# Optimization experiments

Measured on AMD Instinct MI355X. Metric: run time of the kernel, lower is better.

The kernel has to match this reference:

```python
import jax, jax.numpy as jnp
import numpy as np

N_NODES = 100000
N_EDGES = 1000000
D_IN = 64
D_MODEL = 64  # H * D
H = 4
D = D_MODEL // H


def setup_inputs() -> dict:
    key = jax.random.key(0)
    ks = jax.random.split(key, 9)
    nodes = jax.random.normal(ks[0], (N_NODES, D_IN), dtype=jnp.float32)
    senders = jax.random.randint(ks[1], (N_EDGES,), 0, N_NODES, dtype=jnp.int32)
    receivers = jnp.sort(jax.random.randint(ks[2], (N_EDGES,), 0, N_NODES, dtype=jnp.int32))
    s = 1.0 / np.sqrt(D_IN)
    W_qk = jax.random.uniform(ks[3], (D_IN, D_MODEL), jnp.float32, -s, s)
    b_qk = jnp.zeros((D_MODEL,), jnp.float32)
    W_v = jax.random.uniform(ks[4], (D_IN, D_MODEL), jnp.float32, -s, s)
    b_v = jnp.zeros((D_MODEL,), jnp.float32)
    so = 1.0 / np.sqrt(D_MODEL)
    W_out = jax.random.uniform(ks[5], (D_MODEL, D_MODEL), jnp.float32, -so, so)
    b_out = jnp.zeros((D_MODEL,), jnp.float32)
    return {
        'nodes': nodes, 'W_qk': W_qk, 'b_qk': b_qk, 'W_v': W_v, 'b_v': b_v,
        'W_out': W_out, 'b_out': b_out, 'senders': senders, 'receivers': receivers,
    }


def _segment_softmax(logits, segment_ids, num_segments):
    # jraph-style numerically stable segment softmax (segments are sorted)
    maxs = jax.ops.segment_max(logits, segment_ids, num_segments, indices_are_sorted=True)
    e = jnp.exp(logits - maxs[segment_ids])
    z = jax.ops.segment_sum(e, segment_ids, num_segments, indices_are_sorted=True)
    return e / z[segment_ids]


def reference(nodes, W_qk, b_qk, W_v, b_v, W_out, b_out, senders, receivers):
    N = nodes.shape[0]
    # projections: N (H D) -> N H D
    qks = (nodes @ W_qk + b_qk).reshape(N, H, D)
    vs = (nodes @ W_v + b_v).reshape(N, H, D)
    # per-edge QK scores: [E, H]
    scores = jnp.einsum('ehd,ehd->eh', qks[receivers], qks[senders])
    attn = _segment_softmax(scores, receivers, N)
    # weighted message scatter: [E,H,D] -> [N, H*D]
    messages = (attn[..., None] * vs[senders]).reshape(-1, H * D)
    ctx = jax.ops.segment_sum(messages, receivers, N, indices_are_sorted=True)
    out = ctx @ W_out + b_out
    return out, attn
```

## Files before the change

### kernel.cpp

```cpp
#include <hip/hip_runtime.h>
#include <math.h>


#define XS_PAD 68
#define WS_PAD 132

typedef _Float16 h2 __attribute__((ext_vector_type(2)));

__device__ inline unsigned pack2(float a, float b) {
    h2 h = { (_Float16)a, (_Float16)b };
    return __builtin_bit_cast(unsigned, h);
}

__global__ __launch_bounds__(256) void mhga_proj_rowptr(
    const float* __restrict__ X,
    const float* __restrict__ Wqk, const float* __restrict__ bqk,
    const float* __restrict__ Wv,  const float* __restrict__ bv,
    unsigned char* __restrict__ packed,
    const int* __restrict__ receivers, int* __restrict__ row_ptr,
    int N, int E, int PB)
{
    if ((int)blockIdx.x >= PB) {
        const int n = (blockIdx.x - PB) * 256 + threadIdx.x;
        if (n > N) return;
        int lo = 0, hi = E;
        while (lo < hi) {
            const int mid = (lo + hi) >> 1;
            if (receivers[mid] < n) lo = mid + 1; else hi = mid;
        }
        row_ptr[n] = lo;
        return;
    }

    __shared__ float Xs[64 * XS_PAD];
    __shared__ float Ws[64 * WS_PAD];
    const int t = threadIdx.x;
    const int m0 = blockIdx.x * 64;

#pragma unroll
    for (int rep = 0; rep < 4; ++rep) {
        const int idx = t * 4 + rep * 1024;
        const int m = idx >> 6, k = idx & 63;
        float4 xv = make_float4(0.f, 0.f, 0.f, 0.f);
        if (m0 + m < N) xv = *(const float4*)(X + (size_t)(m0 + m) * 64 + k);
        Xs[(k + 0) * XS_PAD + m] = xv.x;
        Xs[(k + 1) * XS_PAD + m] = xv.y;
        Xs[(k + 2) * XS_PAD + m] = xv.z;
        Xs[(k + 3) * XS_PAD + m] = xv.w;
    }
#pragma unroll
    for (int rep = 0; rep < 8; ++rep) {
        const int idx = t * 4 + rep * 1024;
        const int k = idx >> 7, j = idx & 127;
        const float4 wv = (j < 64) ? *(const float4*)(Wqk + k * 64 + j)
                                   : *(const float4*)(Wv + k * 64 + (j - 64));
        *(float4*)(Ws + k * WS_PAD + j) = wv;
    }
    __syncthreads();

    const int tx = t & 15, ty = t >> 4;
    float acc[4][8] = {};
#pragma unroll 8
    for (int k = 0; k < 64; ++k) {
        const float4 a  = *(const float4*)(Xs + k * XS_PAD + ty * 4);
        const float4 b0 = *(const float4*)(Ws + k * WS_PAD + tx * 8);
        const float4 b1 = *(const float4*)(Ws + k * WS_PAD + tx * 8 + 4);
        const float av[4] = {a.x, a.y, a.z, a.w};
        const float bv8[8] = {b0.x, b0.y, b0.z, b0.w, b1.x, b1.y, b1.z, b1.w};
#pragma unroll
        for (int i = 0; i < 4; ++i)
#pragma unroll
            for (int j = 0; j < 8; ++j)
                acc[i][j] = fmaf(av[i], bv8[j], acc[i][j]);
    }

    const bool isV = (tx >= 8);
    const float* bias = isV ? bv : bqk;
    const int j0 = (tx & 7) * 8;
    const int c0 = (tx & 7) * 2;
    const float4 bb0 = *(const float4*)(bias + j0);
    const float4 bb1 = *(const float4*)(bias + j0 + 4);
#pragma unroll
    for (int i = 0; i < 4; ++i) {
        const int m = m0 + ty * 4 + i;
        if (m < N) {
            const unsigned u0 = pack2(acc[i][0] + bb0.x, acc[i][1] + bb0.y);
            const unsigned u1 = pack2(acc[i][2] + bb0.z, acc[i][3] + bb0.w);
            const unsigned u2 = pack2(acc[i][4] + bb1.x, acc[i][5] + bb1.y);
            const unsigned u3 = pack2(acc[i][6] + bb1.z, acc[i][7] + bb1.w);
            unsigned char* row = packed + (size_t)m * 256 + (isV ? 8 : 0);
            *(uint2*)(row + c0 * 16)       = make_uint2(u0, u1);
            *(uint2*)(row + (c0 + 1) * 16) = make_uint2(u2, u3);
        }
    }
}

__global__ __launch_bounds__(256) void mhga_attn(
    const unsigned char* __restrict__ packed,
    const int* __restrict__ senders, const int* __restrict__ row_ptr,
    const float* __restrict__ Wout, const float* __restrict__ bout,
    float* __restrict__ p_ws, float* __restrict__ out,
    float* __restrict__ attn_out, int N)
{
    __shared__ float sW[64 * 64];
    __shared__ float sCtx[4][64];
    const int t = threadIdx.x;
#pragma unroll
    for (int i = t * 4; i < 4096; i += 1024)
        *(float4*)(sW + i) = *(const float4*)(Wout + i);

    const int wave = t >> 6, lane = t & 63;
    const int g = lane >> 4, tl = lane & 15;
    const float bo = bout[lane];
    __syncthreads();

    for (int n0 = blockIdx.x * 4; n0 < N; n0 += gridDim.x * 4) {
        const int n = n0 + wave;
        const bool active = (n < N);
        float l = 0.f;
        float4 ctx = make_float4(0.f, 0.f, 0.f, 0.f);
        int e0 = 0, e1 = 0;

        if (active) {
            e0 = row_ptr[n];
            e1 = row_ptr[n + 1];
            const uint4 qpk = *(const uint4*)(packed + (size_t)n * 256 + tl * 16);
            const h2 q0 = __builtin_bit_cast(h2, qpk.x);
            const h2 q1 = __builtin_bit_cast(h2, qpk.y);

            for (int base = e0; base < e1; base += 64) {
                const int cnt = min(64, e1 - base);
                int sid = 0;
                if (base + lane < e1) sid = senders[base + lane];

                int idx = g;
                int scur = __shfl(sid, idx, 64);
                if (idx >= cnt) scur = 0;
                uint4 pk = *(const uint4*)(packed + (size_t)scur * 256 + tl * 16);

                const int iters = (cnt + 3) >> 2;
                for (int i = 0; i < iters; ++i) {
                    const int nidx = idx + 4;
                    int snxt = __shfl(sid, nidx & 63, 64);
                    if (nidx >= cnt) snxt = 0;
                    const uint4 pknext =
                        *(const uint4*)(packed + (size_t)snxt * 256 + tl * 16);
                    if (idx < cnt) {
                        const h2 k0 = __builtin_bit_cast(h2, pk.x);
                        const h2 k1 = __builtin_bit_cast(h2, pk.y);
                        const h2 v0 = __builtin_bit_cast(h2, pk.z);
                        const h2 v1 = __builtin_bit_cast(h2, pk.w);
                        float d = __builtin_amdgcn_fdot2(q0, k0, 0.f, false);
                        d = __builtin_amdgcn_fdot2(q1, k1, d, false);
                        d += __shfl_xor(d, 1, 64);
                        d += __shfl_xor(d, 2, 64);
                        const float p = __expf(d);
                        if ((tl & 3) == 0)
                            p_ws[(size_t)(base + idx) * 4 + (tl >> 2)] = p;
                        l += p;
                        ctx.x = fmaf(p, (float)v0.x, ctx.x);
                        ctx.y = fmaf(p, (float)v0.y, ctx.y);
                        ctx.z = fmaf(p, (float)v1.x, ctx.z);
                        ctx.w = fmaf(p, (float)v1.y, ctx.w);
                    }
                    pk = pknext;
                    idx = nidx;
                }
            }
#pragma unroll
            for (int mask = 16; mask <= 32; mask <<= 1) {
                l     += __shfl_xor(l, mask, 64);
                ctx.x += __shfl_xor(ctx.x, mask, 64);
                ctx.y += __shfl_xor(ctx.y, mask, 64);
                ctx.z += __shfl_xor(ctx.z, mask, 64);
                ctx.w += __shfl_xor(ctx.w, mask, 64);
            }
            const float inv = (l > 0.f) ? (1.f / l) : 0.f;
            if (g == 0) {
                *(float4*)(&sCtx[wave][tl * 4]) =
                    make_float4(ctx.x * inv, ctx.y * inv, ctx.z * inv, ctx.w * inv);
            }
        }

        __syncthreads();

        if (active) {
            const float lh = __shfl(l, (lane & 3) << 2, 64);
            const float invl = (lh > 0.f) ? (1.f / lh) : 0.f;
            volatile const float* vp = p_ws;
            for (int f = e0 * 4 + lane; f < e1 * 4; f += 64)
                attn_out[f] = vp[f] * invl;

            float acc = bo;
#pragma unroll
            for (int k = 0; k < 64; k += 4) {
                const float4 c = *(const float4*)(&sCtx[wave][k]);
                acc = fmaf(c.x, sW[(k + 0) * 64 + lane], acc);
                acc = fmaf(c.y, sW[(k + 1) * 64 + lane], acc);
                acc = fmaf(c.z, sW[(k + 2) * 64 + lane], acc);
                acc = fmaf(c.w, sW[(k + 3) * 64 + lane], acc);
            }
            out[(size_t)n * 64 + lane] = acc;
        }
    }
}

extern "C" void kernel_launch(void* const* d_in, const int* in_sizes, int n_in,
                              void* d_out, int out_size, void* d_ws, size_t ws_size,
                              hipStream_t stream) {
    const float* nodes   = (const float*)d_in[0];
    const float* W_qk    = (const float*)d_in[1];
    const float* b_qk    = (const float*)d_in[2];
    const float* W_v     = (const float*)d_in[3];
    const float* b_v     = (const float*)d_in[4];
    const float* W_out   = (const float*)d_in[5];
    const float* b_out   = (const float*)d_in[6];
    const int* senders   = (const int*)d_in[7];
    const int* receivers = (const int*)d_in[8];

    const int N = in_sizes[0] / 64;
    const int E = in_sizes[7];

    float* out      = (float*)d_out;
    float* attn_out = out + (size_t)N * 64;

    unsigned char* packed = (unsigned char*)d_ws;
    int*   rowp = (int*)(packed + (size_t)N * 256);
    float* p_ws = (float*)(rowp + (((N + 1) + 3) & ~3));

    const int PB = (N + 63) / 64;
    const int RB = (N + 1 + 255) / 256;
    mhga_proj_rowptr<<<PB + RB, 256, 0, stream>>>(
        nodes, W_qk, b_qk, W_v, b_v, packed, receivers, rowp, N, E, PB);

    mhga_attn<<<2048, 256, 0, stream>>>(packed, senders, rowp,
                                        W_out, b_out, p_ws, out, attn_out, N);
}
```

Measured before the change: 193.9 us.

## Use MFMA for node projection and drop block barrier in attention loop

Rewrites the projection GEMM to convert X and W to fp16 in swizzled shared memory and compute it with 16x16x32 f16 MFMA instructions instead of scalar FMAs. In the attention kernel, the per-iteration __syncthreads is replaced by a waitcnt so waves advance independently, and the software prefetch of the next sender row is removed in favour of a direct load. Inputs are now rounded to fp16 before the matmul, and the output is written with scattered 2-byte stores, so precision and store efficiency may change. Dropping the prefetch may expose more gather latency.

```diff
diff --git a/kernel.cpp b/kernel.cpp
--- a/kernel.cpp
+++ b/kernel.cpp
@@ -2,15 +2,11 @@
 #include <math.h>
 
 
-#define XS_PAD 68
-#define WS_PAD 132
-
 typedef _Float16 h2 __attribute__((ext_vector_type(2)));
-
-__device__ inline unsigned pack2(float a, float b) {
-    h2 h = { (_Float16)a, (_Float16)b };
-    return __builtin_bit_cast(unsigned, h);
-}
+typedef _Float16 half8 __attribute__((ext_vector_type(8)));
+typedef float floatx4 __attribute__((ext_vector_type(4)));
+
+#define WT_PAD 72
 
 __global__ __launch_bounds__(256) void mhga_proj_rowptr(
     const float* __restrict__ X,
@@ -32,8 +28,8 @@
         return;
     }
 
-    __shared__ float Xs[64 * XS_PAD];
-    __shared__ float Ws[64 * WS_PAD];
+    __shared__ __align__(16) _Float16 Xh[64 * WT_PAD];
+    __shared__ __align__(16) _Float16 Wt[128 * WT_PAD];
     const int t = threadIdx.x;
     const int m0 = blockIdx.x * 64;
 
@@ -43,10 +39,11 @@
         const int m = idx >> 6, k = idx & 63;
         float4 xv = make_float4(0.f, 0.f, 0.f, 0.f);
         if (m0 + m < N) xv = *(const float4*)(X + (size_t)(m0 + m) * 64 + k);
-        Xs[(k + 0) * XS_PAD + m] = xv.x;
-        Xs[(k + 1) * XS_PAD + m] = xv.y;
-        Xs[(k + 2) * XS_PAD + m] = xv.z;
-        Xs[(k + 3) * XS_PAD + m] = xv.w;
+        h2 lo = { (_Float16)xv.x, (_Float16)xv.y };
+        h2 hi = { (_Float16)xv.z, (_Float16)xv.w };
+        uint2 u = make_uint2(__builtin_bit_cast(unsigned, lo),
+                             __builtin_bit_cast(unsigned, hi));
+        *(uint2*)(&Xh[m * WT_PAD + k]) = u;
     }
 #pragma unroll
     for (int rep = 0; rep < 8; ++rep) {
@@ -54,43 +51,50 @@
         const int k = idx >> 7, j = idx & 127;
         const float4 wv = (j < 64) ? *(const float4*)(Wqk + k * 64 + j)
                                    : *(const float4*)(Wv + k * 64 + (j - 64));
-        *(float4*)(Ws + k * WS_PAD + j) = wv;
+        const float w4[4] = {wv.x, wv.y, wv.z, wv.w};
+#pragma unroll
+        for (int i = 0; i < 4; ++i) {
+            const int n = j + i;
+            Wt[n * WT_PAD + (k ^ ((n & 7) * 8))] = (_Float16)w4[i];
+        }
     }
     __syncthreads();
 
-    const int tx = t & 15, ty = t >> 4;
-    float acc[4][8] = {};
-#pragma unroll 8
-    for (int k = 0; k < 64; ++k) {
-        const float4 a  = *(const float4*)(Xs + k * XS_PAD + ty * 4);
-        const float4 b0 = *(const float4*)(Ws + k * WS_PAD + tx * 8);
-        const float4 b1 = *(const float4*)(Ws + k * WS_PAD + tx * 8 + 4);
-        const float av[4] = {a.x, a.y, a.z, a.w};
-        const float bv8[8] = {b0.x, b0.y, b0.z, b0.w, b1.x, b1.y, b1.z, b1.w};
-#pragma unroll
-        for (int i = 0; i < 4; ++i)
-#pragma unroll
-            for (int j = 0; j < 8; ++j)
-                acc[i][j] = fmaf(av[i], bv8[j], acc[i][j]);
-    }
-
-    const bool isV = (tx >= 8);
-    const float* bias = isV ? bv : bqk;
-    const int j0 = (tx & 7) * 8;
-    const int c0 = (tx & 7) * 2;
-    const float4 bb0 = *(const float4*)(bias + j0);
-    const float4 bb1 = *(const float4*)(bias + j0 + 4);
-#pragma unroll
-    for (int i = 0; i < 4; ++i) {
-        const int m = m0 + ty * 4 + i;
-        if (m < N) {
-            const unsigned u0 = pack2(acc[i][0] + bb0.x, acc[i][1] + bb0.y);
-            const unsigned u1 = pack2(acc[i][2] + bb0.z, acc[i][3] + bb0.w);
-            const unsigned u2 = pack2(acc[i][4] + bb1.x, acc[i][5] + bb1.y);
-            const unsigned u3 = pack2(acc[i][6] + bb1.z, acc[i][7] + bb1.w);
-            unsigned char* row = packed + (size_t)m * 256 + (isV ? 8 : 0);
-            *(uint2*)(row + c0 * 16)       = make_uint2(u0, u1);
-            *(uint2*)(row + (c0 + 1) * 16) = make_uint2(u2, u3);
+    const int w = t >> 6, lane = t & 63;
+    const int ln = lane & 15, quad = lane >> 4;
+
+    const half8 a0 = *(const half8*)(&Xh[(w * 16 + ln) * WT_PAD + quad * 8]);
+    const half8 a1 = *(const half8*)(&Xh[(w * 16 + ln) * WT_PAD + 32 + quad * 8]);
+
+    float bt[8];
+#pragma unroll
+    for (int tt = 0; tt < 8; ++tt)
+        bt[tt] = (tt < 4) ? bqk[tt * 16 + ln] : bv[(tt - 4) * 16 + ln];
+
+    floatx4 acc[8];
+#pragma unroll
+    for (int tt = 0; tt < 8; ++tt) {
+        const int n = tt * 16 + ln;
+        const int swz = (n & 7);
+        const half8 b0 = *(const half8*)(&Wt[n * WT_PAD + ((quad ^ swz) * 8)]);
+        const half8 b1 = *(const half8*)(&Wt[n * WT_PAD + (((4 + quad) ^ swz) * 8)]);
+        floatx4 c = {0.f, 0.f, 0.f, 0.f};
+        c = __builtin_amdgcn_mfma_f32_16x16x32_f16(a0, b0, c, 0, 0, 0);
+        c = __builtin_amdgcn_mfma_f32_16x16x32_f16(a1, b1, c, 0, 0, 0);
+        acc[tt] = c;
+    }
+
+#pragma unroll
+    for (int tt = 0; tt < 8; ++tt) {
+        const int off = (tt < 4)
+            ? ((tt * 4 + (ln >> 2)) * 16 + (ln & 3) * 2)
+            : (((tt - 4) * 4 + (ln >> 2)) * 16 + 8 + (ln & 3) * 2);
+#pragma unroll
+        for (int r = 0; r < 4; ++r) {
+            const int row = m0 + w * 16 + quad * 4 + r;
+            if (row < N)
+                *(_Float16*)(packed + (size_t)row * 256 + off) =
+                    (_Float16)(acc[tt][r] + bt[tt]);
         }
     }
 }
@@ -114,94 +118,77 @@
     const float bo = bout[lane];
     __syncthreads();
 
-    for (int n0 = blockIdx.x * 4; n0 < N; n0 += gridDim.x * 4) {
-        const int n = n0 + wave;
-        const bool active = (n < N);
+    for (int n = blockIdx.x * 4 + wave; n < N; n += gridDim.x * 4) {
+        const int e0 = row_ptr[n];
+        const int e1 = row_ptr[n + 1];
         float l = 0.f;
         float4 ctx = make_float4(0.f, 0.f, 0.f, 0.f);
-        int e0 = 0, e1 = 0;
-
-        if (active) {
-            e0 = row_ptr[n];
-            e1 = row_ptr[n + 1];
-            const uint4 qpk = *(const uint4*)(packed + (size_t)n * 256 + tl * 16);
-            const h2 q0 = __builtin_bit_cast(h2, qpk.x);
-            const h2 q1 = __builtin_bit_cast(h2, qpk.y);
-
-            for (int base = e0; base < e1; base += 64) {
-                const int cnt = min(64, e1 - base);
-                int sid = 0;
-                if (base + lane < e1) sid = senders[base + lane];
-
-                int idx = g;
-                int scur = __shfl(sid, idx, 64);
-                if (idx >= cnt) scur = 0;
-                uint4 pk = *(const uint4*)(packed + (size_t)scur * 256 + tl * 16);
-
-                const int iters = (cnt + 3) >> 2;
-                for (int i = 0; i < iters; ++i) {
-                    const int nidx = idx + 4;
-                    int snxt = __shfl(sid, nidx & 63, 64);
-                    if (nidx >= cnt) snxt = 0;
-                    const uint4 pknext =
-                        *(const uint4*)(packed + (size_t)snxt * 256 + tl * 16);
-                    if (idx < cnt) {
-                        const h2 k0 = __builtin_bit_cast(h2, pk.x);
-                        const h2 k1 = __builtin_bit_cast(h2, pk.y);
-                        const h2 v0 = __builtin_bit_cast(h2, pk.z);
-                        const h2 v1 = __builtin_bit_cast(h2, pk.w);
-                        float d = __builtin_amdgcn_fdot2(q0, k0, 0.f, false);
-                        d = __builtin_amdgcn_fdot2(q1, k1, d, false);
-                        d += __shfl_xor(d, 1, 64);
-                        d += __shfl_xor(d, 2, 64);
-                        const float p = __expf(d);
-                        if ((tl & 3) == 0)
-                            p_ws[(size_t)(base + idx) * 4 + (tl >> 2)] = p;
-                        l += p;
-                        ctx.x = fmaf(p, (float)v0.x, ctx.x);
-                        ctx.y = fmaf(p, (float)v0.y, ctx.y);
-                        ctx.z = fmaf(p, (float)v1.x, ctx.z);
-                        ctx.w = fmaf(p, (float)v1.y, ctx.w);
-                    }
-                    pk = pknext;
-                    idx = nidx;
+        const uint4 qpk = *(const uint4*)(packed + (size_t)n * 256 + tl * 16);
+        const h2 q0 = __builtin_bit_cast(h2, qpk.x);
+        const h2 q1 = __builtin_bit_cast(h2, qpk.y);
+
+        for (int base = e0; base < e1; base += 64) {
+            const int cnt = min(64, e1 - base);
+            int sid = 0;
+            if (base + lane < e1) sid = senders[base + lane];
+            const int iters = (cnt + 3) >> 2;
+            for (int i = 0; i < iters; ++i) {
+                const int idx = i * 4 + g;
+                const int s = __shfl(sid, idx, 64);
+                if (idx < cnt) {
+                    const uint4 pk =
+                        *(const uint4*)(packed + (size_t)s * 256 + tl * 16);
+                    const h2 k0 = __builtin_bit_cast(h2, pk.x);
+                    const h2 k1 = __builtin_bit_cast(h2, pk.y);
+                    const h2 v0 = __builtin_bit_cast(h2, pk.z);
+                    const h2 v1 = __builtin_bit_cast(h2, pk.w);
+                    float d = __builtin_amdgcn_fdot2(q0, k0, 0.f, false);
+                    d = __builtin_amdgcn_fdot2(q1, k1, d, false);
+                    d += __shfl_xor(d, 1, 64);
+                    d += __shfl_xor(d, 2, 64);
+                    const float p = __expf(d);
+                    if ((tl & 3) == 0)
+                        p_ws[(size_t)(base + idx) * 4 + (tl >> 2)] = p;
+                    l += p;
+                    ctx.x = fmaf(p, (float)v0.x, ctx.x);
+                    ctx.y = fmaf(p, (float)v0.y, ctx.y);
+                    ctx.z = fmaf(p, (float)v1.x, ctx.z);
+                    ctx.w = fmaf(p, (float)v1.y, ctx.w);
                 }
             }
-#pragma unroll
-            for (int mask = 16; mask <= 32; mask <<= 1) {
-                l     += __shfl_xor(l, mask, 64);
-                ctx.x += __shfl_xor(ctx.x, mask, 64);
-                ctx.y += __shfl_xor(ctx.y, mask, 64);
-                ctx.z += __shfl_xor(ctx.z, mask, 64);
-                ctx.w += __shfl_xor(ctx.w, mask, 64);
-            }
-            const float inv = (l > 0.f) ? (1.f / l) : 0.f;
-            if (g == 0) {
-                *(float4*)(&sCtx[wave][tl * 4]) =
-                    make_float4(ctx.x * inv, ctx.y * inv, ctx.z * inv, ctx.w * inv);
-            }
-        }
-
-        __syncthreads();
-
-        if (active) {
-            const float lh = __shfl(l, (lane & 3) << 2, 64);
-            const float invl = (lh > 0.f) ? (1.f / lh) : 0.f;
-            volatile const float* vp = p_ws;
-            for (int f = e0 * 4 + lane; f < e1 * 4; f += 64)
-                attn_out[f] = vp[f] * invl;
-
-            float acc = bo;
-#pragma unroll
-            for (int k = 0; k < 64; k += 4) {
-                const float4 c = *(const float4*)(&sCtx[wave][k]);
-                acc = fmaf(c.x, sW[(k + 0) * 64 + lane], acc);
-                acc = fmaf(c.y, sW[(k + 1) * 64 + lane], acc);
-                acc = fmaf(c.z, sW[(k + 2) * 64 + lane], acc);
-                acc = fmaf(c.w, sW[(k + 3) * 64 + lane], acc);
-            }
-            out[(size_t)n * 64 + lane] = acc;
-        }
+        }
+#pragma unroll
+        for (int mask = 16; mask <= 32; mask <<= 1) {
+            l     += __shfl_xor(l, mask, 64);
+            ctx.x += __shfl_xor(ctx.x, mask, 64);
+            ctx.y += __shfl_xor(ctx.y, mask, 64);
+            ctx.z += __shfl_xor(ctx.z, mask, 64);
+            ctx.w += __shfl_xor(ctx.w, mask, 64);
+        }
+        const float inv = (l > 0.f) ? (1.f / l) : 0.f;
+        if (g == 0) {
+            *(float4*)(&sCtx[wave][tl * 4]) =
+                make_float4(ctx.x * inv, ctx.y * inv, ctx.z * inv, ctx.w * inv);
+        }
+
+        __builtin_amdgcn_s_waitcnt(0x0F70);
+
+        const float lh = __shfl(l, (lane & 3) << 2, 64);
+        const float invl = (lh > 0.f) ? (1.f / lh) : 0.f;
+        volatile const float* vp = p_ws;
+        for (int f = e0 * 4 + lane; f < e1 * 4; f += 64)
+            attn_out[f] = vp[f] * invl;
+
+        float acc = bo;
+#pragma unroll
+        for (int k = 0; k < 64; k += 4) {
+            const float4 c = *(const float4*)(&sCtx[wave][k]);
+            acc = fmaf(c.x, sW[(k + 0) * 64 + lane], acc);
+            acc = fmaf(c.y, sW[(k + 1) * 64 + lane], acc);
+            acc = fmaf(c.z, sW[(k + 2) * 64 + lane], acc);
+            acc = fmaf(c.w, sW[(k + 3) * 64 + lane], acc);
+        }
+        out[(size_t)n * 64 + lane] = acc;
     }
 }
 
```

Measured after the change: 198.7 us. 1.02x slower.
